# Optimization experiments

Measured on AMD Instinct MI355X. Metric: run time of the kernel, lower is better.

## Reference

```python
import jax, jax.numpy as jnp
from jax import lax
import numpy as np

VOCAB = 50000
EMB = 256
HID = 512
NFEAT = 2048
B, T = 128, 64


def setup_inputs() -> dict:
    key = jax.random.key(0)
    ks = jax.random.split(key, 9)
    s_e = 1.0 / np.sqrt(HID)
    return {
        "m": jax.random.randint(ks[0], (B, T), 0, VOCAB, dtype=jnp.int64) if jax.config.jax_enable_x64 else jax.random.randint(ks[0], (B, T), 0, VOCAB, dtype=jnp.int32),
        "images": jax.random.normal(ks[1], (B, NFEAT), dtype=jnp.float32),
        "emb_table": jax.random.normal(ks[2], (VOCAB, EMB), dtype=jnp.float32),
        "W_ih": jax.random.uniform(ks[3], (4 * HID, EMB), jnp.float32, -s_e, s_e),
        "W_hh": jax.random.uniform(ks[4], (4 * HID, HID), jnp.float32, -s_e, s_e),
        "b_ih": jax.random.uniform(ks[5], (4 * HID,), jnp.float32, -s_e, s_e),
        "b_hh": jax.random.uniform(ks[6], (4 * HID,), jnp.float32, -s_e, s_e),
        "W_out": jax.random.uniform(ks[7], (NFEAT, HID), jnp.float32, -s_e, s_e),
        "b_out": jax.random.uniform(ks[8], (NFEAT,), jnp.float32, -s_e, s_e),
    }


def reference(m, images, emb_table, W_ih, W_hh, b_ih, b_hh, W_out, b_out):
    # m: [B, T] int token ids. images is unused by the original forward.
    Bsz = m.shape[0]
    emb = emb_table[m]                                  # [B, T, E]
    # Precompute input projections for all steps (one big GEMM)
    x_proj = jnp.einsum("bte,ge->btg", emb, W_ih) + b_ih  # [B, T, 4H]
    x_proj = jnp.swapaxes(x_proj, 0, 1)                   # [T, B, 4H]

    h0 = jnp.zeros((Bsz, HID), dtype=emb.dtype)
    c0 = jnp.zeros((Bsz, HID), dtype=emb.dtype)

    def step(carry, xg):
        h, c = carry
        gates = xg + h @ W_hh.T + b_hh                  # [B, 4H]
        i, f, g, o = jnp.split(gates, 4, axis=-1)       # PyTorch LSTMCell gate order
        c_new = jax.nn.sigmoid(f) * c + jax.nn.sigmoid(i) * jnp.tanh(g)
        h_new = jax.nn.sigmoid(o) * jnp.tanh(c_new)
        return (h_new, c_new), None

    (h, _), _ = lax.scan(step, (h0, c0), x_proj)
    return h @ W_out.T + b_out                           # [B, NFEAT]
```

## Files before the change

kernel.cpp:

```cpp
#include <hip/hip_runtime.h>
#include <hip/hip_bf16.h>

#define BATCH 128
#define TSTEPS 64
#define EMB 256
#define HID 512
#define GATES 2048
#define NFEAT 2048

typedef __bf16 bf16_t;
typedef __attribute__((ext_vector_type(8))) __bf16 bf16x8;
typedef __attribute__((ext_vector_type(4))) float f32x4;

#define MFMA16 __builtin_amdgcn_mfma_f32_16x16x32_bf16

__device__ __forceinline__ bf16x8 frag16(const bf16_t* __restrict__ base, int row0, int stride,
                                         int k0, int lane) {
    return *(const bf16x8*)(base + (size_t)(row0 + (lane & 15)) * stride + k0 + ((lane >> 4) << 3));
}

__device__ __forceinline__ float sigm(float x) { return 1.f / (1.f + __expf(-x)); }
__device__ __forceinline__ float tanh_f(float x) { return 1.f - 2.f / (__expf(2.f * x) + 1.f); }

__device__ __forceinline__ void ld4_sys_v4(const void* p0, const void* p1,
                                           const void* p2, const void* p3,
                                           uint4& a, uint4& b, uint4& c, uint4& d) {
    asm volatile("global_load_dwordx4 %0, %4, off sc0 sc1\n\t"
                 "global_load_dwordx4 %1, %5, off sc0 sc1\n\t"
                 "global_load_dwordx4 %2, %6, off sc0 sc1\n\t"
                 "global_load_dwordx4 %3, %7, off sc0 sc1\n\t"
                 "s_waitcnt vmcnt(0)"
                 : "=&v"(a), "=&v"(b), "=&v"(c), "=&v"(d)
                 : "v"(p0), "v"(p1), "v"(p2), "v"(p3)
                 : "memory");
}
__device__ __forceinline__ void st_sys_v2(void* p, unsigned lo, unsigned hi) {
    uint2 v = make_uint2(lo, hi);
    asm volatile("global_store_dwordx2 %0, %1, off sc0 sc1" :: "v"(p), "v"(v) : "memory");
}

__device__ __forceinline__ float bflo(unsigned w) {
    return __builtin_bit_cast(float, (w & 0xffffu) << 16);
}
__device__ __forceinline__ float bfhi(unsigned w) {
    return __builtin_bit_cast(float, w & 0xffff0000u);
}
__device__ __forceinline__ unsigned f2bf(float x) {
    return (unsigned)__builtin_bit_cast(unsigned short, (bf16_t)x);
}

__global__ __launch_bounds__(256) void k_prep(
    const float* __restrict__ Wih, const float* __restrict__ Whh, const float* __restrict__ Wout,
    const float* __restrict__ bih, const float* __restrict__ bhh,
    bf16_t* __restrict__ wih_b, bf16_t* __restrict__ whh_b, bf16_t* __restrict__ wout_b,
    float* __restrict__ biassum, unsigned long long* __restrict__ pkt0) {
    const int N1 = GATES * EMB;
    const int N2 = GATES * HID;
    const int N3 = NFEAT * HID;
    const int N4 = GATES;
    const int N5 = 32768;
    const long total = (long)N1 + N2 + N3 + N4 + N5;
    for (long i = (long)blockIdx.x * blockDim.x + threadIdx.x; i < total;
         i += (long)gridDim.x * blockDim.x) {
        long x = i;
        if (x < N1) { wih_b[x] = (bf16_t)Wih[x]; continue; } x -= N1;
        if (x < N2) { whh_b[x] = (bf16_t)Whh[x]; continue; } x -= N2;
        if (x < N3) { wout_b[x] = (bf16_t)Wout[x]; continue; } x -= N3;
        if (x < N4) { biassum[x] = bih[x] + bhh[x]; continue; } x -= N4;
        pkt0[x] = 0ull;
    }
}

__global__ __launch_bounds__(256) void k_xproj(
    const int* __restrict__ m, const float* __restrict__ emb_tab,
    const bf16_t* __restrict__ Wih, const float* __restrict__ biassum,
    bf16_t* __restrict__ xproj) {
    int lane = threadIdx.x & 63, w = threadIdx.x >> 6;
    int t = blockIdx.x;
    int b0 = (w >> 1) * 64;
    int g0 = blockIdx.y * 128 + (w & 1) * 64;
    int q = lane >> 4;
    int tok[4];
    #pragma unroll
    for (int i = 0; i < 4; i++)
        tok[i] = m[(b0 + 16 * i + (lane & 15)) * TSTEPS + t];
    f32x4 acc[4][4] = {};
    #pragma unroll
    for (int k = 0; k < EMB; k += 32) {
        bf16x8 af[4], bf[4];
        #pragma unroll
        for (int i = 0; i < 4; i++) {
            const float* src = emb_tab + (size_t)tok[i] * EMB + k + q * 8;
            float4 lo = *(const float4*)(src);
            float4 hi = *(const float4*)(src + 4);
            bf16x8 v;
            v[0] = (bf16_t)lo.x; v[1] = (bf16_t)lo.y; v[2] = (bf16_t)lo.z; v[3] = (bf16_t)lo.w;
            v[4] = (bf16_t)hi.x; v[5] = (bf16_t)hi.y; v[6] = (bf16_t)hi.z; v[7] = (bf16_t)hi.w;
            af[i] = v;
        }
        #pragma unroll
        for (int j = 0; j < 4; j++) bf[j] = frag16(Wih, g0 + 16 * j, EMB, k, lane);
        #pragma unroll
        for (int i = 0; i < 4; i++)
            #pragma unroll
            for (int j = 0; j < 4; j++)
                acc[i][j] = MFMA16(af[i], bf[j], acc[i][j], 0, 0, 0);
    }
    #pragma unroll
    for (int j = 0; j < 4; j++) {
        int g = g0 + 16 * j + (lane & 15);
        float bs = biassum[g];
        #pragma unroll
        for (int i = 0; i < 4; i++)
            #pragma unroll
            for (int r = 0; r < 4; r++) {
                int row = t * BATCH + b0 + 16 * i + (q << 2) + r;
                xproj[(size_t)row * GATES + g] = (bf16_t)(acc[i][j][r] + bs);
            }
    }
}

__global__ __launch_bounds__(512, 1) void k_rnn(
    const bf16_t* __restrict__ xp,
    const bf16_t* __restrict__ whh,
    char* __restrict__ hbuf,
    bf16_t* __restrict__ hfin) {
    __shared__ __align__(16) char hstage[16384];
    __shared__ float gex[4][16][66];
    const int tid = threadIdx.x;
    const int lane = tid & 63, w = tid >> 6;
    const int group = blockIdx.x >> 3;
    const int s     = blockIdx.x & 7;
    const int g = w >> 1, hh = w & 1;

    bf16x8 Bf0[16], Bf1[16];
    {
        const bf16_t* wb = whh + (size_t)(g * HID + s * 64 + hh * 32) * HID;
        #pragma unroll
        for (int kt = 0; kt < 16; ++kt) {
            Bf0[kt] = frag16(wb, 0, HID, kt * 32, lane);
            Bf1[kt] = frag16(wb, 16, HID, kt * 32, lane);
        }
        #pragma unroll
        for (int kt = 0; kt < 16; ++kt)
            asm volatile("" : "+v"(Bf0[kt]), "+v"(Bf1[kt]));
    }

    const int r_up = tid >> 5;
    const int c0 = (tid & 31) * 2;
    float cst0 = 0.f, cst1 = 0.f;

    size_t pk_off;
    int fin_idx;
    {
        int j = s * 64 + c0;
        int kt = j >> 5;
        int lane_p = (((j & 31) >> 3) << 4) | r_up;
        int dw = kt * 256 + lane_p * 4 + ((j & 7) >> 1);
        pk_off = (size_t)group * 32768 + (size_t)dw * 8;
        fin_idx = dw;
    }
    const char* q0base = hbuf + (size_t)group * 32768 + (size_t)tid * 32;
    const char* q2base = hbuf + (size_t)group * 32768 + (size_t)(tid + 512) * 32;

    int parS = 0;
    for (int t = 0; t < TSTEPS; ++t) {
        unsigned xw0, xw1, xw2, xw3;
        {
            const bf16_t* xrow = xp + ((size_t)t * BATCH + group * 16 + r_up) * GATES + s * 64 + c0;
            xw0 = *(const unsigned*)(xrow);
            xw1 = *(const unsigned*)(xrow + HID);
            xw2 = *(const unsigned*)(xrow + 2 * HID);
            xw3 = *(const unsigned*)(xrow + 3 * HID);
        }

        {
            const char* q0 = q0base + (size_t)parS * 262144;
            const char* q2 = q2base + (size_t)parS * 262144;
            const unsigned tg = (unsigned)t;
            uint4 a, b, c, d;
            do {
                ld4_sys_v4(q0, q0 + 16, q2, q2 + 16, a, b, c, d);
            } while (!__all((int)(a.y == tg && a.w == tg && b.y == tg && b.w == tg &&
                                  c.y == tg && c.w == tg && d.y == tg && d.w == tg)));
            *(uint4*)(hstage + (size_t)tid * 16)         = make_uint4(a.x, a.z, b.x, b.z);
            *(uint4*)(hstage + (size_t)(tid + 512) * 16) = make_uint4(c.x, c.z, d.x, d.z);
        }
        __syncthreads();

        f32x4 a0 = {}, a1 = {};
        {
            const bf16_t* hs = (const bf16_t*)hstage;
            #pragma unroll
            for (int kt = 0; kt < 16; ++kt) {
                bf16x8 a = *(const bf16x8*)(hs + kt * 512 + lane * 8);
                a0 = MFMA16(a, Bf0[kt], a0, 0, 0, 0);
                a1 = MFMA16(a, Bf1[kt], a1, 0, 0, 0);
            }
        }

        {
            const int jj = lane & 15, q = lane >> 4;
            #pragma unroll
            for (int rr = 0; rr < 4; ++rr) {
                gex[g][q * 4 + rr][hh * 32 + jj]      = a0[rr];
                gex[g][q * 4 + rr][hh * 32 + 16 + jj] = a1[rr];
            }
        }
        __syncthreads();

        {
            float2 gi = *(const float2*)&gex[0][r_up][c0];
            float2 gf = *(const float2*)&gex[1][r_up][c0];
            float2 gg = *(const float2*)&gex[2][r_up][c0];
            float2 go = *(const float2*)&gex[3][r_up][c0];
            float iv0 = gi.x + bflo(xw0), iv1 = gi.y + bfhi(xw0);
            float fv0 = gf.x + bflo(xw1), fv1 = gf.y + bfhi(xw1);
            float gv0 = gg.x + bflo(xw2), gv1 = gg.y + bfhi(xw2);
            float ov0 = go.x + bflo(xw3), ov1 = go.y + bfhi(xw3);
            cst0 = sigm(fv0) * cst0 + sigm(iv0) * tanh_f(gv0);
            cst1 = sigm(fv1) * cst1 + sigm(iv1) * tanh_f(gv1);
            float h0v = sigm(ov0) * tanh_f(cst0);
            float h1v = sigm(ov1) * tanh_f(cst1);
            unsigned pack = f2bf(h0v) | (f2bf(h1v) << 16);
            int parD = parS ^ 1;
            st_sys_v2(hbuf + (size_t)parD * 262144 + pk_off, pack, (unsigned)(t + 1));
            if (t == TSTEPS - 1)
                *((unsigned*)hfin + (size_t)group * 4096 + fin_idx) = pack;
            parS = parD;
        }
    }
}

__device__ __forceinline__ bf16x8 frag_piece(const bf16_t* hb, int group, int kt, int lane) {
    return *(const bf16x8*)(hb + (size_t)group * 8192 + kt * 512 + lane * 8);
}

__global__ __launch_bounds__(256) void k_out(
    const bf16_t* __restrict__ h,
    const bf16_t* __restrict__ Wout,
    const float* __restrict__ bout,
    float* __restrict__ out) {
    int lane = threadIdx.x & 63, w = threadIdx.x >> 6;
    int r0 = blockIdx.x * 32 + (w & 1) * 16;
    int g0 = blockIdx.y * 128 + (w >> 1) * 64;
    int group = r0 >> 4;
    f32x4 acc[4] = {};
    #pragma unroll 4
    for (int kt = 0; kt < 16; ++kt) {
        bf16x8 a = frag_piece(h, group, kt, lane);
        #pragma unroll
        for (int t = 0; t < 4; t++) {
            bf16x8 b = frag16(Wout, g0 + 16 * t, HID, kt * 32, lane);
            acc[t] = MFMA16(a, b, acc[t], 0, 0, 0);
        }
    }
    #pragma unroll
    for (int t = 0; t < 4; t++) {
        int g = g0 + 16 * t + (lane & 15);
        float bs = bout[g];
        #pragma unroll
        for (int r = 0; r < 4; r++) {
            int row = r0 + ((lane >> 4) << 2) + r;
            out[(size_t)row * NFEAT + g] = acc[t][r] + bs;
        }
    }
}

extern "C" void kernel_launch(void* const* d_in, const int* in_sizes, int n_in,
                              void* d_out, int out_size, void* d_ws, size_t ws_size,
                              hipStream_t stream) {
    const int*   m       = (const int*)d_in[0];
    const float* emb_tab = (const float*)d_in[2];
    const float* W_ih    = (const float*)d_in[3];
    const float* W_hh    = (const float*)d_in[4];
    const float* b_ih    = (const float*)d_in[5];
    const float* b_hh    = (const float*)d_in[6];
    const float* W_out   = (const float*)d_in[7];
    const float* b_out   = (const float*)d_in[8];

    char* ws = (char*)d_ws;
    bf16_t* xpb     = (bf16_t*)(ws + 0);
    bf16_t* wih_b   = (bf16_t*)(ws + 33554432);
    bf16_t* whh_b   = (bf16_t*)(ws + 34603008);
    bf16_t* wout_b  = (bf16_t*)(ws + 36700160);
    char*   hbuf    = (char*)  (ws + 38797312);
    bf16_t* hfin    = (bf16_t*)(ws + 39321600);
    float*  biassum = (float*) (ws + 39452672);

    k_prep<<<dim3(1024), dim3(256), 0, stream>>>(W_ih, W_hh, W_out, b_ih, b_hh,
                                                 wih_b, whh_b, wout_b, biassum,
                                                 (unsigned long long*)hbuf);

    k_xproj<<<dim3(64, 16), dim3(256), 0, stream>>>(m, emb_tab, wih_b, biassum, xpb);

    k_rnn<<<dim3(64), dim3(512), 0, stream>>>(xpb, whh_b, hbuf, hfin);

    k_out<<<dim3(4, 16), dim3(256), 0, stream>>>(hfin, wout_b, b_out, (float*)d_out);
}
```

Measured before the change: 291.0 us.

## Process four batch groups per RNN block with software-pipelined packet loads

The recurrent kernel now launches 16 blocks instead of 64, and each block interleaves four batch groups. While one group computes, the h-packet and x-projection loads for the other groups are already in flight through a two-slot prefetch scheme, and __syncthreads is replaced by hand-placed waitcnt and barrier calls. The aim is to hide the cross-block polling latency of the sequential recurrence behind other groups' compute. In exchange each block does four times the serial work per step and the machine runs with fewer active CUs.

Measured after the change: 558.4 us. 1.92x slower.

```diff
diff --git a/kernel.cpp b/kernel.cpp
--- a/kernel.cpp
+++ b/kernel.cpp
@@ -7,6 +7,7 @@
 #define HID 512
 #define GATES 2048
 #define NFEAT 2048
+#define GPB 4
 
 typedef __bf16 bf16_t;
 typedef __attribute__((ext_vector_type(8))) __bf16 bf16x8;
@@ -22,31 +23,57 @@
 __device__ __forceinline__ float sigm(float x) { return 1.f / (1.f + __expf(-x)); }
 __device__ __forceinline__ float tanh_f(float x) { return 1.f - 2.f / (__expf(2.f * x) + 1.f); }
 
-__device__ __forceinline__ void ld4_sys_v4(const void* p0, const void* p1,
-                                           const void* p2, const void* p3,
-                                           uint4& a, uint4& b, uint4& c, uint4& d) {
-    asm volatile("global_load_dwordx4 %0, %4, off sc0 sc1\n\t"
-                 "global_load_dwordx4 %1, %5, off sc0 sc1\n\t"
-                 "global_load_dwordx4 %2, %6, off sc0 sc1\n\t"
-                 "global_load_dwordx4 %3, %7, off sc0 sc1\n\t"
-                 "s_waitcnt vmcnt(0)"
-                 : "=&v"(a), "=&v"(b), "=&v"(c), "=&v"(d)
-                 : "v"(p0), "v"(p1), "v"(p2), "v"(p3)
-                 : "memory");
-}
+__device__ __forceinline__ float bflo(unsigned w) {
+    return __builtin_bit_cast(float, (w & 0xffffu) << 16);
+}
+__device__ __forceinline__ float bfhi(unsigned w) {
+    return __builtin_bit_cast(float, w & 0xffff0000u);
+}
+__device__ __forceinline__ unsigned f2bf(float x) {
+    return (unsigned)__builtin_bit_cast(unsigned short, (bf16_t)x);
+}
+
 __device__ __forceinline__ void st_sys_v2(void* p, unsigned lo, unsigned hi) {
     uint2 v = make_uint2(lo, hi);
     asm volatile("global_store_dwordx2 %0, %1, off sc0 sc1" :: "v"(p), "v"(v) : "memory");
 }
 
-__device__ __forceinline__ float bflo(unsigned w) {
-    return __builtin_bit_cast(float, (w & 0xffffu) << 16);
-}
-__device__ __forceinline__ float bfhi(unsigned w) {
-    return __builtin_bit_cast(float, w & 0xffff0000u);
-}
-__device__ __forceinline__ unsigned f2bf(float x) {
-    return (unsigned)__builtin_bit_cast(unsigned short, (bf16_t)x);
+struct Slot { uint4 a, b, c, d; unsigned x0, x1, x2, x3; };
+
+__device__ __forceinline__ void issue_slot(Slot& S, const void* q0, const void* q2,
+                                           const void* xr) {
+    asm volatile(
+        "global_load_dwordx4 %0, %8, off sc0 sc1\n\t"
+        "global_load_dwordx4 %1, %8, off offset:16 sc0 sc1\n\t"
+        "global_load_dwordx4 %2, %9, off sc0 sc1\n\t"
+        "global_load_dwordx4 %3, %9, off offset:16 sc0 sc1\n\t"
+        "global_load_dword %4, %10, off\n\t"
+        "global_load_dword %5, %10, off offset:1024\n\t"
+        "global_load_dword %6, %10, off offset:2048\n\t"
+        "global_load_dword %7, %10, off offset:3072"
+        : "=&v"(S.a), "=&v"(S.b), "=&v"(S.c), "=&v"(S.d),
+          "=&v"(S.x0), "=&v"(S.x1), "=&v"(S.x2), "=&v"(S.x3)
+        : "v"(q0), "v"(q2), "v"(xr)
+        : "memory");
+}
+
+__device__ __forceinline__ void reload_pkts(Slot& S, const void* q0, const void* q2) {
+    asm volatile(
+        "global_load_dwordx4 %0, %4, off sc0 sc1\n\t"
+        "global_load_dwordx4 %1, %4, off offset:16 sc0 sc1\n\t"
+        "global_load_dwordx4 %2, %5, off sc0 sc1\n\t"
+        "global_load_dwordx4 %3, %5, off offset:16 sc0 sc1\n\t"
+        "s_waitcnt vmcnt(0)"
+        : "=&v"(S.a), "=&v"(S.b), "=&v"(S.c), "=&v"(S.d)
+        : "v"(q0), "v"(q2)
+        : "memory");
+}
+
+__device__ __forceinline__ void bar_lds() {
+    __builtin_amdgcn_sched_barrier(0);
+    asm volatile("s_waitcnt lgkmcnt(0)" ::: "memory");
+    __builtin_amdgcn_s_barrier();
+    __builtin_amdgcn_sched_barrier(0);
 }
 
 __global__ __launch_bounds__(256) void k_prep(
@@ -129,8 +156,8 @@
     __shared__ float gex[4][16][66];
     const int tid = threadIdx.x;
     const int lane = tid & 63, w = tid >> 6;
-    const int group = blockIdx.x >> 3;
-    const int s     = blockIdx.x & 7;
+    const int s   = blockIdx.x & 7;
+    const int set = blockIdx.x >> 3;
     const int g = w >> 1, hh = w & 1;
 
     bf16x8 Bf0[16], Bf1[16];
@@ -148,88 +175,93 @@
 
     const int r_up = tid >> 5;
     const int c0 = (tid & 31) * 2;
-    float cst0 = 0.f, cst1 = 0.f;
-
-    size_t pk_off;
-    int fin_idx;
+    float cst[GPB][2] = {};
+
+    int pk8;
     {
         int j = s * 64 + c0;
         int kt = j >> 5;
         int lane_p = (((j & 31) >> 3) << 4) | r_up;
-        int dw = kt * 256 + lane_p * 4 + ((j & 7) >> 1);
-        pk_off = (size_t)group * 32768 + (size_t)dw * 8;
-        fin_idx = dw;
-    }
-    const char* q0base = hbuf + (size_t)group * 32768 + (size_t)tid * 32;
-    const char* q2base = hbuf + (size_t)group * 32768 + (size_t)(tid + 512) * 32;
-
-    int parS = 0;
-    for (int t = 0; t < TSTEPS; ++t) {
-        unsigned xw0, xw1, xw2, xw3;
-        {
-            const bf16_t* xrow = xp + ((size_t)t * BATCH + group * 16 + r_up) * GATES + s * 64 + c0;
-            xw0 = *(const unsigned*)(xrow);
-            xw1 = *(const unsigned*)(xrow + HID);
-            xw2 = *(const unsigned*)(xrow + 2 * HID);
-            xw3 = *(const unsigned*)(xrow + 3 * HID);
-        }
-
-        {
-            const char* q0 = q0base + (size_t)parS * 262144;
-            const char* q2 = q2base + (size_t)parS * 262144;
-            const unsigned tg = (unsigned)t;
-            uint4 a, b, c, d;
-            do {
-                ld4_sys_v4(q0, q0 + 16, q2, q2 + 16, a, b, c, d);
-            } while (!__all((int)(a.y == tg && a.w == tg && b.y == tg && b.w == tg &&
-                                  c.y == tg && c.w == tg && d.y == tg && d.w == tg)));
-            *(uint4*)(hstage + (size_t)tid * 16)         = make_uint4(a.x, a.z, b.x, b.z);
-            *(uint4*)(hstage + (size_t)(tid + 512) * 16) = make_uint4(c.x, c.z, d.x, d.z);
-        }
-        __syncthreads();
-
-        f32x4 a0 = {}, a1 = {};
-        {
-            const bf16_t* hs = (const bf16_t*)hstage;
-            #pragma unroll
-            for (int kt = 0; kt < 16; ++kt) {
-                bf16x8 a = *(const bf16x8*)(hs + kt * 512 + lane * 8);
-                a0 = MFMA16(a, Bf0[kt], a0, 0, 0, 0);
-                a1 = MFMA16(a, Bf1[kt], a1, 0, 0, 0);
-            }
-        }
-
-        {
-            const int jj = lane & 15, q = lane >> 4;
-            #pragma unroll
-            for (int rr = 0; rr < 4; ++rr) {
-                gex[g][q * 4 + rr][hh * 32 + jj]      = a0[rr];
-                gex[g][q * 4 + rr][hh * 32 + 16 + jj] = a1[rr];
-            }
-        }
-        __syncthreads();
-
-        {
-            float2 gi = *(const float2*)&gex[0][r_up][c0];
-            float2 gf = *(const float2*)&gex[1][r_up][c0];
-            float2 gg = *(const float2*)&gex[2][r_up][c0];
-            float2 go = *(const float2*)&gex[3][r_up][c0];
-            float iv0 = gi.x + bflo(xw0), iv1 = gi.y + bfhi(xw0);
-            float fv0 = gf.x + bflo(xw1), fv1 = gf.y + bfhi(xw1);
-            float gv0 = gg.x + bflo(xw2), gv1 = gg.y + bfhi(xw2);
-            float ov0 = go.x + bflo(xw3), ov1 = go.y + bfhi(xw3);
-            cst0 = sigm(fv0) * cst0 + sigm(iv0) * tanh_f(gv0);
-            cst1 = sigm(fv1) * cst1 + sigm(iv1) * tanh_f(gv1);
-            float h0v = sigm(ov0) * tanh_f(cst0);
-            float h1v = sigm(ov1) * tanh_f(cst1);
-            unsigned pack = f2bf(h0v) | (f2bf(h1v) << 16);
-            int parD = parS ^ 1;
-            st_sys_v2(hbuf + (size_t)parD * 262144 + pk_off, pack, (unsigned)(t + 1));
-            if (t == TSTEPS - 1)
-                *((unsigned*)hfin + (size_t)group * 4096 + fin_idx) = pack;
-            parS = parD;
-        }
-    }
+        pk8 = (kt * 256 + lane_p * 4 + ((j & 7) >> 1)) * 8;
+    }
+
+    Slot slot0, slot1;
+
+#define PKQ0(T_, PH) ((const void*)(hbuf + (((T_) & 1) ? 262144 : 0) \
+                      + (size_t)((set * GPB + (PH)) * 32768) + (size_t)tid * 32))
+#define PKQ2(T_, PH) ((const void*)(hbuf + (((T_) & 1) ? 262144 : 0) \
+                      + (size_t)((set * GPB + (PH)) * 32768) + (size_t)(tid + 512) * 32))
+#define XRP(T_, PH)  ((const void*)(xp + ((size_t)((T_) * BATCH + (set * GPB + (PH)) * 16 + r_up)) * GATES \
+                      + s * 64 + c0))
+
+    issue_slot(slot0, PKQ0(0, 0), PKQ2(0, 0), XRP(0, 0));
+    issue_slot(slot1, PKQ0(0, 1), PKQ2(0, 1), XRP(0, 1));
+
+#define PHASE(IDX, VM, T_) do {                                                            \
+    Slot& S = ((IDX) & 1) ? slot1 : slot0;                                                 \
+    asm volatile("s_waitcnt vmcnt(%0)" :: "i"(VM) : "memory");                             \
+    __builtin_amdgcn_sched_barrier(0);                                                     \
+    { unsigned tg = (unsigned)(T_);                                                        \
+      while (!(S.a.y == tg && S.a.w == tg && S.b.y == tg && S.b.w == tg &&                 \
+               S.c.y == tg && S.c.w == tg && S.d.y == tg && S.d.w == tg))                  \
+          reload_pkts(S, PKQ0(T_, IDX), PKQ2(T_, IDX)); }                                  \
+    unsigned xv0 = S.x0, xv1 = S.x1, xv2 = S.x2, xv3 = S.x3;                               \
+    *(uint4*)(hstage + (size_t)tid * 16) = make_uint4(S.a.x, S.a.z, S.b.x, S.b.z);         \
+    *(uint4*)(hstage + (size_t)(tid + 512) * 16) = make_uint4(S.c.x, S.c.z, S.d.x, S.d.z); \
+    { const int pt = ((IDX) + 2) & 3;                                                      \
+      const int tt = ((IDX) < 2) ? (T_) : ((T_) + 1);                                      \
+      issue_slot(S, PKQ0(tt, pt), PKQ2(tt, pt), XRP(tt, pt)); }                            \
+    bar_lds();                                                       \
+    f32x4 a0 = {}, a1 = {};                                                                \
+    { const bf16_t* hs = (const bf16_t*)hstage;                                            \
+      _Pragma("unroll")                                                                    \
+      for (int kt = 0; kt < 16; ++kt) {                                                    \
+          bf16x8 av = *(const bf16x8*)(hs + kt * 512 + lane * 8);                          \
+          a0 = MFMA16(av, Bf0[kt], a0, 0, 0, 0);                                           \
+          a1 = MFMA16(av, Bf1[kt], a1, 0, 0, 0);                                           \
+      } }                                                                                  \
+    { const int jj = lane & 15, qq = lane >> 4;                                            \
+      _Pragma("unroll")                                                                    \
+      for (int rr = 0; rr < 4; ++rr) {                                                     \
+          gex[g][qq * 4 + rr][hh * 32 + jj]      = a0[rr];                                 \
+          gex[g][qq * 4 + rr][hh * 32 + 16 + jj] = a1[rr];                                 \
+      } }                                                                                  \
+    bar_lds();                                         \
+    { float2 gi = *(const float2*)&gex[0][r_up][c0];                                       \
+      float2 gf = *(const float2*)&gex[1][r_up][c0];                                       \
+      float2 gg2 = *(const float2*)&gex[2][r_up][c0];                                      \
+      float2 go = *(const float2*)&gex[3][r_up][c0];                                       \
+      float iv0 = gi.x + bflo(xv0), iv1 = gi.y + bfhi(xv0);                                \
+      float fv0 = gf.x + bflo(xv1), fv1 = gf.y + bfhi(xv1);                                \
+      float gv0 = gg2.x + bflo(xv2), gv1 = gg2.y + bfhi(xv2);                              \
+      float ov0 = go.x + bflo(xv3), ov1 = go.y + bfhi(xv3);                                \
+      cst[IDX][0] = sigm(fv0) * cst[IDX][0] + sigm(iv0) * tanh_f(gv0);                     \
+      cst[IDX][1] = sigm(fv1) * cst[IDX][1] + sigm(iv1) * tanh_f(gv1);                     \
+      float h0v = sigm(ov0) * tanh_f(cst[IDX][0]);                                         \
+      float h1v = sigm(ov1) * tanh_f(cst[IDX][1]);                                         \
+      unsigned pack = f2bf(h0v) | (f2bf(h1v) << 16);                                       \
+      char* pst = hbuf + ((((T_) + 1) & 1) ? 262144 : 0)                                   \
+                + (size_t)((set * GPB + (IDX)) * 32768) + pk8;                             \
+      st_sys_v2(pst, pack, (unsigned)((T_) + 1));                                          \
+      if ((T_) == TSTEPS - 1)                                                              \
+          *((unsigned*)hfin + ((size_t)(set * GPB + (IDX)) << 12) + (pk8 >> 3)) = pack;    \
+    }                                                                                      \
+} while (0)
+
+    PHASE(0, 8, 0);
+    PHASE(1, 9, 0);
+    PHASE(2, 10, 0);
+    PHASE(3, 10, 0);
+    for (int t = 1; t < TSTEPS; ++t) {
+        PHASE(0, 10, t);
+        PHASE(1, 10, t);
+        PHASE(2, 10, t);
+        PHASE(3, 10, t);
+    }
+#undef PHASE
+#undef PKQ0
+#undef PKQ2
+#undef XRP
 }
 
 __device__ __forceinline__ bf16x8 frag_piece(const bf16_t* hb, int group, int kt, int lane) {
@@ -294,7 +326,7 @@
 
     k_xproj<<<dim3(64, 16), dim3(256), 0, stream>>>(m, emb_tab, wih_b, biassum, xpb);
 
-    k_rnn<<<dim3(64), dim3(512), 0, stream>>>(xpb, whh_b, hbuf, hfin);
+    k_rnn<<<dim3(16), dim3(512), 0, stream>>>(xpb, whh_b, hbuf, hfin);
 
     k_out<<<dim3(4, 16), dim3(256), 0, stream>>>(hfin, wout_b, b_out, (float*)d_out);
 }
```

## Drop prep kernel, fuse weight casts, restructure LSTM recurrence with per-wave flags

Applied to the files above, without the earlier changes.

Removes the separate weight-conversion prep kernel and converts fp32 weights to bf16 inline where they are loaded (xproj, rnn, out), with the bias sum done in xproj. The recurrent kernel now uses 256 threads, each wave computing all four gates for 16 hidden units, so gate math happens in registers without the LDS exchange and one of the two barriers. Cross-block sync changes from polling tagged data words to per-wave flag counters polled by one wave, and the first step is specialised since h0 is zero. Per-step costs are lower, but the flag protocol adds an extra global round trip, and more weight registers per wave risks register pressure.

New measurement: 332.0 us. +14.1%, slower.

```diff
diff --git a/kernel.cpp b/kernel.cpp
--- a/kernel.cpp
+++ b/kernel.cpp
@@ -18,10 +18,37 @@
                                          int k0, int lane) {
     return *(const bf16x8*)(base + (size_t)(row0 + (lane & 15)) * stride + k0 + ((lane >> 4) << 3));
 }
+__device__ __forceinline__ bf16x8 frag16f(const float* __restrict__ base, int row0, int stride,
+                                          int k0, int lane) {
+    const float* p = base + (size_t)(row0 + (lane & 15)) * stride + k0 + ((lane >> 4) << 3);
+    float4 lo = *(const float4*)p;
+    float4 hi = *(const float4*)(p + 4);
+    bf16x8 v;
+    v[0] = (bf16_t)lo.x; v[1] = (bf16_t)lo.y; v[2] = (bf16_t)lo.z; v[3] = (bf16_t)lo.w;
+    v[4] = (bf16_t)hi.x; v[5] = (bf16_t)hi.y; v[6] = (bf16_t)hi.z; v[7] = (bf16_t)hi.w;
+    return v;
+}
 
 __device__ __forceinline__ float sigm(float x) { return 1.f / (1.f + __expf(-x)); }
 __device__ __forceinline__ float tanh_f(float x) { return 1.f - 2.f / (__expf(2.f * x) + 1.f); }
 
+__device__ __forceinline__ float bfbits2f(unsigned b16) {
+    return __builtin_bit_cast(float, b16 << 16);
+}
+__device__ __forceinline__ unsigned f2bf(float x) {
+    return (unsigned)__builtin_bit_cast(unsigned short, (bf16_t)x);
+}
+
+__device__ __forceinline__ unsigned ld_sys(const unsigned* p) {
+    return __hip_atomic_load(p, __ATOMIC_RELAXED, __HIP_MEMORY_SCOPE_SYSTEM);
+}
+__device__ __forceinline__ void st_sys(unsigned* p, unsigned v) {
+    __hip_atomic_store(p, v, __ATOMIC_RELAXED, __HIP_MEMORY_SCOPE_SYSTEM);
+}
+__device__ __forceinline__ void st_sys_v2(void* p, unsigned lo, unsigned hi) {
+    uint2 v = make_uint2(lo, hi);
+    asm volatile("global_store_dwordx2 %0, %1, off sc0 sc1" :: "v"(p), "v"(v) : "memory");
+}
 __device__ __forceinline__ void ld4_sys_v4(const void* p0, const void* p1,
                                            const void* p2, const void* p3,
                                            uint4& a, uint4& b, uint4& c, uint4& d) {
@@ -34,47 +61,14 @@
                  : "v"(p0), "v"(p1), "v"(p2), "v"(p3)
                  : "memory");
 }
-__device__ __forceinline__ void st_sys_v2(void* p, unsigned lo, unsigned hi) {
-    uint2 v = make_uint2(lo, hi);
-    asm volatile("global_store_dwordx2 %0, %1, off sc0 sc1" :: "v"(p), "v"(v) : "memory");
-}
-
-__device__ __forceinline__ float bflo(unsigned w) {
-    return __builtin_bit_cast(float, (w & 0xffffu) << 16);
-}
-__device__ __forceinline__ float bfhi(unsigned w) {
-    return __builtin_bit_cast(float, w & 0xffff0000u);
-}
-__device__ __forceinline__ unsigned f2bf(float x) {
-    return (unsigned)__builtin_bit_cast(unsigned short, (bf16_t)x);
-}
-
-__global__ __launch_bounds__(256) void k_prep(
-    const float* __restrict__ Wih, const float* __restrict__ Whh, const float* __restrict__ Wout,
-    const float* __restrict__ bih, const float* __restrict__ bhh,
-    bf16_t* __restrict__ wih_b, bf16_t* __restrict__ whh_b, bf16_t* __restrict__ wout_b,
-    float* __restrict__ biassum, unsigned long long* __restrict__ pkt0) {
-    const int N1 = GATES * EMB;
-    const int N2 = GATES * HID;
-    const int N3 = NFEAT * HID;
-    const int N4 = GATES;
-    const int N5 = 32768;
-    const long total = (long)N1 + N2 + N3 + N4 + N5;
-    for (long i = (long)blockIdx.x * blockDim.x + threadIdx.x; i < total;
-         i += (long)gridDim.x * blockDim.x) {
-        long x = i;
-        if (x < N1) { wih_b[x] = (bf16_t)Wih[x]; continue; } x -= N1;
-        if (x < N2) { whh_b[x] = (bf16_t)Whh[x]; continue; } x -= N2;
-        if (x < N3) { wout_b[x] = (bf16_t)Wout[x]; continue; } x -= N3;
-        if (x < N4) { biassum[x] = bih[x] + bhh[x]; continue; } x -= N4;
-        pkt0[x] = 0ull;
-    }
-}
 
 __global__ __launch_bounds__(256) void k_xproj(
     const int* __restrict__ m, const float* __restrict__ emb_tab,
-    const bf16_t* __restrict__ Wih, const float* __restrict__ biassum,
-    bf16_t* __restrict__ xproj) {
+    const float* __restrict__ Wih, const float* __restrict__ bih, const float* __restrict__ bhh,
+    bf16_t* __restrict__ xproj, unsigned* __restrict__ flags) {
+    if (blockIdx.x == 0 && blockIdx.y == 0 && threadIdx.x < 256)
+        st_sys(flags + threadIdx.x, 0u);
+
     int lane = threadIdx.x & 63, w = threadIdx.x >> 6;
     int t = blockIdx.x;
     int b0 = (w >> 1) * 64;
@@ -99,7 +93,7 @@
             af[i] = v;
         }
         #pragma unroll
-        for (int j = 0; j < 4; j++) bf[j] = frag16(Wih, g0 + 16 * j, EMB, k, lane);
+        for (int j = 0; j < 4; j++) bf[j] = frag16f(Wih, g0 + 16 * j, EMB, k, lane);
         #pragma unroll
         for (int i = 0; i < 4; i++)
             #pragma unroll
@@ -109,7 +103,7 @@
     #pragma unroll
     for (int j = 0; j < 4; j++) {
         int g = g0 + 16 * j + (lane & 15);
-        float bs = biassum[g];
+        float bs = bih[g] + bhh[g];
         #pragma unroll
         for (int i = 0; i < 4; i++)
             #pragma unroll
@@ -120,115 +114,112 @@
     }
 }
 
-__global__ __launch_bounds__(512, 1) void k_rnn(
+__global__ __launch_bounds__(256, 1) void k_rnn(
     const bf16_t* __restrict__ xp,
-    const bf16_t* __restrict__ whh,
+    const float* __restrict__ whh,
     char* __restrict__ hbuf,
-    bf16_t* __restrict__ hfin) {
+    unsigned* __restrict__ flags) {
     __shared__ __align__(16) char hstage[16384];
-    __shared__ float gex[4][16][66];
     const int tid = threadIdx.x;
     const int lane = tid & 63, w = tid >> 6;
     const int group = blockIdx.x >> 3;
     const int s     = blockIdx.x & 7;
-    const int g = w >> 1, hh = w & 1;
-
-    bf16x8 Bf0[16], Bf1[16];
+    const int jj = lane & 15, q = lane >> 4;
+
+    bf16x8 W0[16], W1[16], W2[16], W3[16];
+    #pragma unroll
+    for (int kt = 0; kt < 16; ++kt) {
+        W0[kt] = frag16f(whh, 0 * HID + s * 64 + w * 16, HID, kt * 32, lane);
+        W1[kt] = frag16f(whh, 1 * HID + s * 64 + w * 16, HID, kt * 32, lane);
+        W2[kt] = frag16f(whh, 2 * HID + s * 64 + w * 16, HID, kt * 32, lane);
+        W3[kt] = frag16f(whh, 3 * HID + s * 64 + w * 16, HID, kt * 32, lane);
+    }
+    #pragma unroll
+    for (int kt = 0; kt < 16; ++kt)
+        asm volatile("" : "+v"(W0[kt]), "+v"(W1[kt]), "+v"(W2[kt]), "+v"(W3[kt]));
+
+    const int j0 = s * 64 + w * 16 + q * 4;
+    const size_t pk_off = (size_t)group * 16384 + (size_t)(j0 >> 5) * 1024
+                        + (size_t)((((j0 & 31) >> 3) << 4) | jj) * 16 + (size_t)(q & 1) * 8;
+    unsigned* myflag = flags + group * 32 + s * 4 + w;
+    const unsigned* pollp = flags + group * 32 + (lane & 31);
+
+    float cst[4] = {0.f, 0.f, 0.f, 0.f};
+
     {
-        const bf16_t* wb = whh + (size_t)(g * HID + s * 64 + hh * 32) * HID;
+        const bf16_t* xrow = xp + ((size_t)(group * 16 + jj)) * GATES + j0;
+        uint2 xg[4];
+        #pragma unroll
+        for (int g = 0; g < 4; ++g) xg[g] = *(const uint2*)(xrow + g * HID);
+        unsigned lo = 0, hi = 0;
+        #pragma unroll
+        for (int rr = 0; rr < 4; ++rr) {
+            unsigned sh = (rr & 1) * 16;
+            float iv = bfbits2f(((rr < 2 ? xg[0].x : xg[0].y) >> sh) & 0xffffu);
+            float fv = bfbits2f(((rr < 2 ? xg[1].x : xg[1].y) >> sh) & 0xffffu);
+            float gv = bfbits2f(((rr < 2 ? xg[2].x : xg[2].y) >> sh) & 0xffffu);
+            float ov = bfbits2f(((rr < 2 ? xg[3].x : xg[3].y) >> sh) & 0xffffu);
+            float cn = sigm(iv) * tanh_f(gv);
+            cst[rr] = cn;
+            unsigned hb = f2bf(sigm(ov) * tanh_f(cn));
+            if (rr < 2) lo |= hb << sh; else hi |= hb << sh;
+        }
+        st_sys_v2(hbuf + 131072  + pk_off, lo, hi);
+        asm volatile("s_waitcnt vmcnt(0)" ::: "memory");
+        if (lane == 0) st_sys(myflag, 1u);
+    }
+
+    for (int t = 1; t < TSTEPS; ++t) {
+        const bf16_t* xrow = xp + ((size_t)(t * BATCH + group * 16 + jj)) * GATES + j0;
+        uint2 xg[4];
+        #pragma unroll
+        for (int g = 0; g < 4; ++g) xg[g] = *(const uint2*)(xrow + g * HID);
+
+        if (w == 0) {
+            unsigned v;
+            do { v = ld_sys(pollp); } while (!__all((int)(v >= (unsigned)t)));
+        }
+        __syncthreads();
+
+        {
+            const char* src = hbuf + (size_t)(t & 1) * 131072 + (size_t)group * 16384;
+            uint4 a, b, c, d;
+            ld4_sys_v4(src + (size_t)tid * 16, src + (size_t)(tid + 256) * 16,
+                       src + (size_t)(tid + 512) * 16, src + (size_t)(tid + 768) * 16,
+                       a, b, c, d);
+            *(uint4*)(hstage + (size_t)tid * 16)         = a;
+            *(uint4*)(hstage + (size_t)(tid + 256) * 16) = b;
+            *(uint4*)(hstage + (size_t)(tid + 512) * 16) = c;
+            *(uint4*)(hstage + (size_t)(tid + 768) * 16) = d;
+        }
+        __syncthreads();
+
+        f32x4 a0 = {}, a1 = {}, a2 = {}, a3 = {};
         #pragma unroll
         for (int kt = 0; kt < 16; ++kt) {
-            Bf0[kt] = frag16(wb, 0, HID, kt * 32, lane);
-            Bf1[kt] = frag16(wb, 16, HID, kt * 32, lane);
-        }
-        #pragma unroll
-        for (int kt = 0; kt < 16; ++kt)
-            asm volatile("" : "+v"(Bf0[kt]), "+v"(Bf1[kt]));
-    }
-
-    const int r_up = tid >> 5;
-    const int c0 = (tid & 31) * 2;
-    float cst0 = 0.f, cst1 = 0.f;
-
-    size_t pk_off;
-    int fin_idx;
-    {
-        int j = s * 64 + c0;
-        int kt = j >> 5;
-        int lane_p = (((j & 31) >> 3) << 4) | r_up;
-        int dw = kt * 256 + lane_p * 4 + ((j & 7) >> 1);
-        pk_off = (size_t)group * 32768 + (size_t)dw * 8;
-        fin_idx = dw;
-    }
-    const char* q0base = hbuf + (size_t)group * 32768 + (size_t)tid * 32;
-    const char* q2base = hbuf + (size_t)group * 32768 + (size_t)(tid + 512) * 32;
-
-    int parS = 0;
-    for (int t = 0; t < TSTEPS; ++t) {
-        unsigned xw0, xw1, xw2, xw3;
-        {
-            const bf16_t* xrow = xp + ((size_t)t * BATCH + group * 16 + r_up) * GATES + s * 64 + c0;
-            xw0 = *(const unsigned*)(xrow);
-            xw1 = *(const unsigned*)(xrow + HID);
-            xw2 = *(const unsigned*)(xrow + 2 * HID);
-            xw3 = *(const unsigned*)(xrow + 3 * HID);
-        }
-
-        {
-            const char* q0 = q0base + (size_t)parS * 262144;
-            const char* q2 = q2base + (size_t)parS * 262144;
-            const unsigned tg = (unsigned)t;
-            uint4 a, b, c, d;
-            do {
-                ld4_sys_v4(q0, q0 + 16, q2, q2 + 16, a, b, c, d);
-            } while (!__all((int)(a.y == tg && a.w == tg && b.y == tg && b.w == tg &&
-                                  c.y == tg && c.w == tg && d.y == tg && d.w == tg)));
-            *(uint4*)(hstage + (size_t)tid * 16)         = make_uint4(a.x, a.z, b.x, b.z);
-            *(uint4*)(hstage + (size_t)(tid + 512) * 16) = make_uint4(c.x, c.z, d.x, d.z);
-        }
-        __syncthreads();
-
-        f32x4 a0 = {}, a1 = {};
-        {
-            const bf16_t* hs = (const bf16_t*)hstage;
-            #pragma unroll
-            for (int kt = 0; kt < 16; ++kt) {
-                bf16x8 a = *(const bf16x8*)(hs + kt * 512 + lane * 8);
-                a0 = MFMA16(a, Bf0[kt], a0, 0, 0, 0);
-                a1 = MFMA16(a, Bf1[kt], a1, 0, 0, 0);
-            }
-        }
-
-        {
-            const int jj = lane & 15, q = lane >> 4;
-            #pragma unroll
-            for (int rr = 0; rr < 4; ++rr) {
-                gex[g][q * 4 + rr][hh * 32 + jj]      = a0[rr];
-                gex[g][q * 4 + rr][hh * 32 + 16 + jj] = a1[rr];
-            }
-        }
-        __syncthreads();
-
-        {
-            float2 gi = *(const float2*)&gex[0][r_up][c0];
-            float2 gf = *(const float2*)&gex[1][r_up][c0];
-            float2 gg = *(const float2*)&gex[2][r_up][c0];
-            float2 go = *(const float2*)&gex[3][r_up][c0];
-            float iv0 = gi.x + bflo(xw0), iv1 = gi.y + bfhi(xw0);
-            float fv0 = gf.x + bflo(xw1), fv1 = gf.y + bfhi(xw1);
-            float gv0 = gg.x + bflo(xw2), gv1 = gg.y + bfhi(xw2);
-            float ov0 = go.x + bflo(xw3), ov1 = go.y + bfhi(xw3);
-            cst0 = sigm(fv0) * cst0 + sigm(iv0) * tanh_f(gv0);
-            cst1 = sigm(fv1) * cst1 + sigm(iv1) * tanh_f(gv1);
-            float h0v = sigm(ov0) * tanh_f(cst0);
-            float h1v = sigm(ov1) * tanh_f(cst1);
-            unsigned pack = f2bf(h0v) | (f2bf(h1v) << 16);
-            int parD = parS ^ 1;
-            st_sys_v2(hbuf + (size_t)parD * 262144 + pk_off, pack, (unsigned)(t + 1));
-            if (t == TSTEPS - 1)
-                *((unsigned*)hfin + (size_t)group * 4096 + fin_idx) = pack;
-            parS = parD;
-        }
+            bf16x8 hb = *(const bf16x8*)(hstage + kt * 1024 + lane * 16);
+            a0 = MFMA16(W0[kt], hb, a0, 0, 0, 0);
+            a1 = MFMA16(W1[kt], hb, a1, 0, 0, 0);
+            a2 = MFMA16(W2[kt], hb, a2, 0, 0, 0);
+            a3 = MFMA16(W3[kt], hb, a3, 0, 0, 0);
+        }
+
+        unsigned lo = 0, hi = 0;
+        #pragma unroll
+        for (int rr = 0; rr < 4; ++rr) {
+            unsigned sh = (rr & 1) * 16;
+            float iv = a0[rr] + bfbits2f(((rr < 2 ? xg[0].x : xg[0].y) >> sh) & 0xffffu);
+            float fv = a1[rr] + bfbits2f(((rr < 2 ? xg[1].x : xg[1].y) >> sh) & 0xffffu);
+            float gv = a2[rr] + bfbits2f(((rr < 2 ? xg[2].x : xg[2].y) >> sh) & 0xffffu);
+            float ov = a3[rr] + bfbits2f(((rr < 2 ? xg[3].x : xg[3].y) >> sh) & 0xffffu);
+            float cn = sigm(fv) * cst[rr] + sigm(iv) * tanh_f(gv);
+            cst[rr] = cn;
+            unsigned hb = f2bf(sigm(ov) * tanh_f(cn));
+            if (rr < 2) lo |= hb << sh; else hi |= hb << sh;
+        }
+        st_sys_v2(hbuf + (size_t)((t + 1) & 1) * 131072 + pk_off, lo, hi);
+        asm volatile("s_waitcnt vmcnt(0)" ::: "memory");
+        if (lane == 0) st_sys(myflag, (unsigned)(t + 1));
     }
 }
 
@@ -238,7 +229,7 @@
 
 __global__ __launch_bounds__(256) void k_out(
     const bf16_t* __restrict__ h,
-    const bf16_t* __restrict__ Wout,
+    const float* __restrict__ Wout,
     const float* __restrict__ bout,
     float* __restrict__ out) {
     int lane = threadIdx.x & 63, w = threadIdx.x >> 6;
@@ -251,7 +242,7 @@
         bf16x8 a = frag_piece(h, group, kt, lane);
         #pragma unroll
         for (int t = 0; t < 4; t++) {
-            bf16x8 b = frag16(Wout, g0 + 16 * t, HID, kt * 32, lane);
+            bf16x8 b = frag16f(Wout, g0 + 16 * t, HID, kt * 32, lane);
             acc[t] = MFMA16(a, b, acc[t], 0, 0, 0);
         }
     }
@@ -280,21 +271,14 @@
     const float* b_out   = (const float*)d_in[8];
 
     char* ws = (char*)d_ws;
-    bf16_t* xpb     = (bf16_t*)(ws + 0);
-    bf16_t* wih_b   = (bf16_t*)(ws + 33554432);
-    bf16_t* whh_b   = (bf16_t*)(ws + 34603008);
-    bf16_t* wout_b  = (bf16_t*)(ws + 36700160);
-    char*   hbuf    = (char*)  (ws + 38797312);
-    bf16_t* hfin    = (bf16_t*)(ws + 39321600);
-    float*  biassum = (float*) (ws + 39452672);
-
-    k_prep<<<dim3(1024), dim3(256), 0, stream>>>(W_ih, W_hh, W_out, b_ih, b_hh,
-                                                 wih_b, whh_b, wout_b, biassum,
-                                                 (unsigned long long*)hbuf);
-
-    k_xproj<<<dim3(64, 16), dim3(256), 0, stream>>>(m, emb_tab, wih_b, biassum, xpb);
-
-    k_rnn<<<dim3(64), dim3(512), 0, stream>>>(xpb, whh_b, hbuf, hfin);
-
-    k_out<<<dim3(4, 16), dim3(256), 0, stream>>>(hfin, wout_b, b_out, (float*)d_out);
-}
+    bf16_t*   xpb   = (bf16_t*)  (ws + 0);
+    char*     hbuf  = (char*)    (ws + 33554432);
+    unsigned* flags = (unsigned*)(ws + 33816576);
+
+    k_xproj<<<dim3(64, 16), dim3(256), 0, stream>>>(m, emb_tab, W_ih, b_ih, b_hh, xpb, flags);
+
+    k_rnn<<<dim3(64), dim3(256), 0, stream>>>(xpb, W_hh, hbuf, flags);
+
+    k_out<<<dim3(4, 16), dim3(256), 0, stream>>>((const bf16_t*)hbuf, W_out, b_out,
+                                                 (float*)d_out);
+}
```
